# Optimization experiments

Hardware: AMD Instinct MI355X
Metric: run time of the kernel (lower is better)

Reference implementation:

```python
import jax, jax.numpy as jnp
import numpy as np

IN, OUT, IO, CF, CS = 128, 128, 512, 512, 1024
B = 8192
TAU_IO, TAU_CF, TAU_CS = 2.0, 5.0, 70.0


def _lin(x, W, b):
    # torch nn.Linear: y = x @ W.T + b, W has shape [out, in]
    return x @ W.T + b


def setup_inputs() -> dict:
    key = jax.random.key(0)
    ks = jax.random.split(key, 24)

    def wb(i, fan_out, fan_in):
        s = 1.0 / np.sqrt(fan_in)
        W = jax.random.uniform(ks[2 * i], (fan_out, fan_in), jnp.float32, -s, s)
        b = jax.random.uniform(ks[2 * i + 1], (fan_out,), jnp.float32, -s, s)
        return W, b

    Wi2io, bi2io = wb(0, IO, IN)
    Wio2o, bio2o = wb(1, OUT, IO)
    Wio2io, bio2io = wb(2, IO, IO)
    Wio2cf, bio2cf = wb(3, CF, IO)
    Wcf2io, bcf2io = wb(4, IO, CF)
    Wcf2cs, bcf2cs = wb(5, CS, CF)
    Wcf2cf, bcf2cf = wb(6, CF, CF)
    Wcs2cf, bcs2cf = wb(7, CF, CS)
    Wcs2cs, bcs2cs = wb(8, CS, CS)

    x = jax.random.normal(ks[18], (B, IN), jnp.float32)
    io_state = jnp.zeros((B, IO), jnp.float32)
    cf_state = jnp.zeros((B, CF), jnp.float32)
    cs_state = jnp.zeros((B, CS), jnp.float32)

    return dict(
        x=x, io_state=io_state, cf_state=cf_state, cs_state=cs_state,
        Wi2io=Wi2io, bi2io=bi2io, Wio2o=Wio2o, bio2o=bio2o,
        Wio2io=Wio2io, bio2io=bio2io, Wio2cf=Wio2cf, bio2cf=bio2cf,
        Wcf2io=Wcf2io, bcf2io=bcf2io, Wcf2cs=Wcf2cs, bcf2cs=bcf2cs,
        Wcf2cf=Wcf2cf, bcf2cf=bcf2cf, Wcs2cf=Wcs2cf, bcs2cf=bcs2cf,
        Wcs2cs=Wcs2cs, bcs2cs=bcs2cs,
    )


def reference(x, io_state, cf_state, cs_state,
              Wi2io, bi2io, Wio2o, bio2o,
              Wio2io, bio2io, Wio2cf, bio2cf,
              Wcf2io, bcf2io, Wcf2cs, bcf2cs,
              Wcf2cf, bcf2cf, Wcs2cf, bcs2cf,
              Wcs2cs, bcs2cs):
    x = x.reshape(-1, IN)
    # leaky-integrated updates; all branches read the *previous* states
    io_new = jnp.tanh(
        (1.0 - 1.0 / TAU_IO) * io_state
        + (_lin(io_state, Wio2io, bio2io)
           + _lin(cf_state, Wcf2io, bcf2io)
           + _lin(x, Wi2io, bi2io)) / TAU_IO)
    cf_new = jnp.tanh(
        (1.0 - 1.0 / TAU_CF) * cf_state
        + (_lin(cf_state, Wcf2cf, bcf2cf)
           + _lin(cs_state, Wcs2cf, bcs2cf)
           + _lin(io_state, Wio2cf, bio2cf)) / TAU_CF)
    cs_new = jnp.tanh(
        (1.0 - 1.0 / TAU_CS) * cs_state
        + (_lin(cs_state, Wcs2cs, bcs2cs)
           + _lin(cf_state, Wcf2cs, bcf2cs)) / TAU_CS)
    y = jnp.tanh(_lin(io_new, Wio2o, bio2o))
    return y
```

## Files before the change

### kernel.cpp

```cpp
#include <hip/hip_runtime.h>


typedef float f32x4 __attribute__((ext_vector_type(4)));
typedef __bf16 bf16x4 __attribute__((ext_vector_type(4)));
typedef __bf16 bf16x8 __attribute__((ext_vector_type(8)));
typedef unsigned short u16x4 __attribute__((ext_vector_type(4)));

__device__ __forceinline__ unsigned short f2bf(float f) {
    unsigned u = __builtin_bit_cast(unsigned, f);
    u += 0x7FFFu + ((u >> 16) & 1u);
    return (unsigned short)(u >> 16);
}

__device__ __forceinline__ float tanh_fast(float x) {
    float e = __expf(2.0f * x);
    return 1.0f - 2.0f * __builtin_amdgcn_rcpf(e + 1.0f);
}

__device__ __forceinline__ void gload16(const void* g, void* l) {
    __builtin_amdgcn_global_load_lds(
        (const __attribute__((address_space(1))) void*)g,
        (__attribute__((address_space(3))) void*)l, 16, 0, 0);
}

#define WAITB(N) asm volatile("s_waitcnt vmcnt(" #N ")\n\ts_barrier" ::: "memory")

__device__ __forceinline__ int swz_ad(int row, int k, int L) {
    return row * L + (k & ~63) + ((((k >> 3) & 7) ^ (row & 7)) << 3) + (k & 7);
}

__global__ __launch_bounds__(256) void k_prep(
    const float* __restrict__ x, const float* __restrict__ io,
    const float* __restrict__ cf,
    const float* __restrict__ Wi2io, const float* __restrict__ Wio2io,
    const float* __restrict__ Wcf2io, const float* __restrict__ Wio2o,
    const float* __restrict__ b1, const float* __restrict__ b2,
    const float* __restrict__ b3,
    unsigned short* __restrict__ abf16, unsigned short* __restrict__ wcat,
    unsigned short* __restrict__ w2s, float* __restrict__ bsum)
{
    int idx = blockIdx.x * 256 + threadIdx.x;
    if (idx < 1179648) {
        int m = idx / 144;
        int k = (idx - m * 144) * 8;
        const float* s;
        if (k < 128)      s = x  + m * 128 + k;
        else if (k < 640) s = io + m * 512 + (k - 128);
        else              s = cf + m * 512 + (k - 640);
        f32x4 v0 = *(const f32x4*)s;
        f32x4 v1 = *(const f32x4*)(s + 4);
        bf16x4 h0 = __builtin_convertvector(v0, bf16x4);
        bf16x4 h1 = __builtin_convertvector(v1, bf16x4);
        *(bf16x8*)(abf16 + swz_ad(m, k, 1152)) =
            __builtin_shufflevector(h0, h1, 0,1,2,3,4,5,6,7);
    } else if (idx < 1253376) {
        int q = idx - 1179648;
        int n = q / 144;
        int k = (q - n * 144) * 8;
        const float* s;
        if (k < 128)      s = Wi2io  + n * 128 + k;
        else if (k < 640) s = Wio2io + n * 512 + (k - 128);
        else              s = Wcf2io + n * 512 + (k - 640);
        f32x4 v0 = *(const f32x4*)s;
        f32x4 v1 = *(const f32x4*)(s + 4);
        float w[8];
        #pragma unroll
        for (int t = 0; t < 4; ++t) { w[t] = 0.5f * v0[t]; w[t+4] = 0.5f * v1[t]; }
        #pragma unroll
        for (int t = 0; t < 8; ++t) {
            int kk = k + t;
            if (kk >= 128 && kk < 640 && (kk - 128) == n) w[t] += 0.5f;
        }
        unsigned short* dst = wcat + swz_ad(n, k, 1152);
        #pragma unroll
        for (int t = 0; t < 8; ++t) dst[t] = f2bf(w[t]);
    } else if (idx < 1261568) {
        int q = idx - 1253376;
        int n = q >> 6;
        int k = (q & 63) * 8;
        f32x4 v0 = *(const f32x4*)(Wio2o + n * 512 + k);
        f32x4 v1 = *(const f32x4*)(Wio2o + n * 512 + k + 4);
        bf16x4 h0 = __builtin_convertvector(v0, bf16x4);
        bf16x4 h1 = __builtin_convertvector(v1, bf16x4);
        *(bf16x8*)(w2s + swz_ad(n, k, 512)) =
            __builtin_shufflevector(h0, h1, 0,1,2,3,4,5,6,7);
    } else if (idx < 1262080) {
        int n = idx - 1261568;
        bsum[n] = 0.5f * (b1[n] + b2[n] + b3[n]);
    }
}

__global__ __launch_bounds__(512, 2) void k_gemm1(
    const unsigned short* __restrict__ abf16,
    const unsigned short* __restrict__ wcat,
    const float* __restrict__ bsum,
    unsigned short* __restrict__ ionew)
{
    __shared__ __align__(16) char lds[3][32768];

    const int tid = threadIdx.x, b = blockIdx.x;
    const int xcd = b & 7, idx = b >> 3;
    const int m0 = ((xcd << 3) | (idx & 7)) << 7;
    const int n0 = (idx >> 3) << 7;

    const int lane = tid & 63, wid = tid >> 6;
    const int li = lane & 15, lh = lane >> 4;
    const int wm = (wid >> 1) << 5;
    const int wn = (wid & 1) << 6;

    int a_off[2], b_off[2];
    #pragma unroll
    for (int j = 0; j < 2; ++j) {
        int ra = (wid << 4) + (j << 3) + (lane >> 3);
        a_off[j] = (m0 + ra) * 1152 + ((lane & 7) << 3);
        int rb = (wid << 4) + (j << 3) + (lane >> 3);
        b_off[j] = (n0 + rb) * 1152 + ((lane & 7) << 3);
    }
    const int adst = wid << 11;

    f32x4 zz = {0.f, 0.f, 0.f, 0.f};
    f32x4 acc[2][4];
    #pragma unroll
    for (int i = 0; i < 2; ++i)
        #pragma unroll
        for (int j = 0; j < 4; ++j) acc[i][j] = zz;

#define STAGE1(KT, BUF) do {                                                   \
        int K_ = (KT);                                                         \
        char* A_ = (BUF); char* B_ = (BUF) + 16384;                            \
        const unsigned short* ap = abf16 + (K_ << 6);                          \
        gload16(ap + a_off[0], A_ + adst);                                     \
        gload16(ap + a_off[1], A_ + adst + 1024);                              \
        const unsigned short* wp = wcat + (K_ << 6);                           \
        gload16(wp + b_off[0], B_ + adst);                                     \
        gload16(wp + b_off[1], B_ + adst + 1024);                              \
    } while (0)

#define COMPUTE1(BUF) do {                                                     \
        const char* A_ = (BUF); const char* B_ = (BUF) + 16384;                \
        _Pragma("unroll")                                                      \
        for (int ks = 0; ks < 2; ++ks) {                                       \
            int c = ks * 4 + lh;                                               \
            bf16x8 af[2];                                                      \
            _Pragma("unroll")                                                  \
            for (int mi = 0; mi < 2; ++mi) {                                   \
                int r = wm + mi * 16 + li;                                     \
                af[mi] = *(const bf16x8*)(A_ + r * 128 + ((c ^ (r & 7)) << 4));\
            }                                                                  \
            _Pragma("unroll")                                                  \
            for (int nj = 0; nj < 4; ++nj) {                                   \
                int rb = wn + nj * 16 + li;                                    \
                bf16x8 bv = *(const bf16x8*)(B_ + rb * 128 +                   \
                                             ((c ^ (rb & 7)) << 4));           \
                acc[0][nj] = __builtin_amdgcn_mfma_f32_16x16x32_bf16(          \
                    af[0], bv, acc[0][nj], 0, 0, 0);                           \
                acc[1][nj] = __builtin_amdgcn_mfma_f32_16x16x32_bf16(          \
                    af[1], bv, acc[1][nj], 0, 0, 0);                           \
            }                                                                  \
        }                                                                      \
    } while (0)

    STAGE1(0, lds[0]);
    STAGE1(1, lds[1]);
    char* p0 = lds[0]; char* p1 = lds[1]; char* p2 = lds[2];
    #pragma unroll 1
    for (int t = 0; t < 18; ++t) {
        if (t < 17) { WAITB(4); } else { WAITB(0); }
        if (t + 2 < 18) STAGE1(t + 2, p2);
        COMPUTE1(p0);
        char* tmp = p0; p0 = p1; p1 = p2; p2 = tmp;
    }
#undef STAGE1
#undef COMPUTE1

    #pragma unroll
    for (int nj = 0; nj < 4; ++nj) {
        int gn = n0 + wn + nj * 16 + li;
        float bb = bsum[gn];
        #pragma unroll
        for (int mi = 0; mi < 2; ++mi) {
            #pragma unroll
            for (int r = 0; r < 4; ++r) {
                int gm = m0 + wm + mi * 16 + (lh << 2) + r;
                float v = tanh_fast(acc[mi][nj][r] + bb);
                ionew[swz_ad(gm, gn, 512)] = f2bf(v);
            }
        }
    }
}

__global__ __launch_bounds__(256, 2) void k_gemm2(
    const unsigned short* __restrict__ ionew,
    const unsigned short* __restrict__ w2s,
    const float* __restrict__ b4,
    float* __restrict__ out)
{
    __shared__ __align__(16) char lds[3][20480];

    const int tid = threadIdx.x, b = blockIdx.x;
    const int xcd = b & 7, idx = b >> 3;
    const int m0 = ((xcd << 5) | idx) << 5;

    const int lane = tid & 63, wid = tid >> 6;
    const int li = lane & 15, lh = lane >> 4;
    const int wn = wid << 5;

    const int a2_off = (m0 + (wid << 3) + (lane >> 3)) * 512 + ((lane & 7) << 3);
    int b2_off[4];
    #pragma unroll
    for (int j = 0; j < 4; ++j)
        b2_off[j] = ((wid << 5) + 8 * j + (lane >> 3)) * 512 + ((lane & 7) << 3);

    f32x4 zz = {0.f, 0.f, 0.f, 0.f};
    f32x4 acc[2][2];
    acc[0][0] = zz; acc[0][1] = zz; acc[1][0] = zz; acc[1][1] = zz;

#define STAGE2(KT, BUF) do {                                                   \
        int K_ = (KT);                                                         \
        char* A_ = (BUF); char* B_ = (BUF) + 4096;                             \
        gload16(ionew + a2_off + (K_ << 6), A_ + (wid << 10));                 \
        _Pragma("unroll")                                                      \
        for (int j = 0; j < 4; ++j)                                            \
            gload16(w2s + b2_off[j] + (K_ << 6), B_ + (wid << 12) + j * 1024); \
    } while (0)

#define COMPUTE2(BUF) do {                                                     \
        const char* A_ = (BUF); const char* B_ = (BUF) + 4096;                 \
        _Pragma("unroll")                                                      \
        for (int ks = 0; ks < 2; ++ks) {                                       \
            int c = ks * 4 + lh;                                               \
            bf16x8 av[2];                                                      \
            _Pragma("unroll")                                                  \
            for (int mi = 0; mi < 2; ++mi) {                                   \
                int r = mi * 16 + li;                                          \
                av[mi] = *(const bf16x8*)(A_ + r * 128 + ((c ^ (r & 7)) << 4));\
            }                                                                  \
            _Pragma("unroll")                                                  \
            for (int nj = 0; nj < 2; ++nj) {                                   \
                int rb = wn + nj * 16 + li;                                    \
                bf16x8 bv = *(const bf16x8*)(B_ + rb * 128 +                   \
                                             ((c ^ (rb & 7)) << 4));           \
                acc[0][nj] = __builtin_amdgcn_mfma_f32_16x16x32_bf16(          \
                    av[0], bv, acc[0][nj], 0, 0, 0);                           \
                acc[1][nj] = __builtin_amdgcn_mfma_f32_16x16x32_bf16(          \
                    av[1], bv, acc[1][nj], 0, 0, 0);                           \
            }                                                                  \
        }                                                                      \
    } while (0)

    STAGE2(0, lds[0]);
    STAGE2(1, lds[1]);
    char* p0 = lds[0]; char* p1 = lds[1]; char* p2 = lds[2];
    #pragma unroll 1
    for (int t = 0; t < 7; ++t) {
        WAITB(5);
        if (t + 2 < 8) STAGE2(t + 2, p2);
        COMPUTE2(p0);
        char* tmp = p0; p0 = p1; p1 = p2; p2 = tmp;
    }
    WAITB(0);
    COMPUTE2(p0);
#undef STAGE2
#undef COMPUTE2

    #pragma unroll
    for (int nj = 0; nj < 2; ++nj) {
        int n = wn + nj * 16 + li;
        float bb = b4[n];
        #pragma unroll
        for (int mi = 0; mi < 2; ++mi) {
            #pragma unroll
            for (int r = 0; r < 4; ++r) {
                int gm = m0 + mi * 16 + (lh << 2) + r;
                out[(size_t)gm * 128 + n] = tanh_fast(acc[mi][nj][r] + bb);
            }
        }
    }
}

extern "C" void kernel_launch(void* const* d_in, const int* in_sizes, int n_in,
                              void* d_out, int out_size, void* d_ws, size_t ws_size,
                              hipStream_t stream)
{
    const float* x      = (const float*)d_in[0];
    const float* io     = (const float*)d_in[1];
    const float* cf     = (const float*)d_in[2];
    const float* Wi2io  = (const float*)d_in[4];
    const float* bi2io  = (const float*)d_in[5];
    const float* Wio2o  = (const float*)d_in[6];
    const float* bio2o  = (const float*)d_in[7];
    const float* Wio2io = (const float*)d_in[8];
    const float* bio2io = (const float*)d_in[9];
    const float* Wcf2io = (const float*)d_in[12];
    const float* bcf2io = (const float*)d_in[13];
    float* out = (float*)d_out;

    char* ws = (char*)d_ws;
    unsigned short* abf16 = (unsigned short*)ws;
    unsigned short* wcat  = (unsigned short*)(ws + 18874368);
    unsigned short* w2s   = (unsigned short*)(ws + 20054016);
    float*          bsum  = (float*)(ws + 20185088);
    unsigned short* ionew = (unsigned short*)(ws + 20187136);

    hipLaunchKernelGGL(k_prep, dim3(4930), dim3(256), 0, stream,
                       x, io, cf, Wi2io, Wio2io, Wcf2io, Wio2o,
                       bi2io, bio2io, bcf2io, abf16, wcat, w2s, bsum);
    hipLaunchKernelGGL(k_gemm1, dim3(256), dim3(512), 0, stream,
                       abf16, wcat, bsum, ionew);
    hipLaunchKernelGGL(k_gemm2, dim3(256), dim3(256), 0, stream,
                       ionew, w2s, bio2o, out);
}
```

Before: 33.47 us.

## Pre-layout B weights in MFMA fragment order and load directly to registers

The prep kernel now writes the concatenated io weight matrix in a per-fragment layout, so each lane can load its MFMA B operand with one 16-byte global load. The GEMM1 kernel stops staging B through LDS, halves its LDS buffers, and loads B fragments into registers each K-step. It also raises wave priority around the MFMA block. This cuts LDS traffic and the B-side LDS reads, but B loads now go to global/L2 with no LDS sharing between waves, and their latency is exposed inside each iteration.

```diff
diff --git a/kernel.cpp b/kernel.cpp
--- a/kernel.cpp
+++ b/kernel.cpp
@@ -36,7 +36,7 @@
     const float* __restrict__ Wcf2io, const float* __restrict__ Wio2o,
     const float* __restrict__ b1, const float* __restrict__ b2,
     const float* __restrict__ b3,
-    unsigned short* __restrict__ abf16, unsigned short* __restrict__ wcat,
+    unsigned short* __restrict__ abf16, unsigned short* __restrict__ wfrag,
     unsigned short* __restrict__ w2s, float* __restrict__ bsum)
 {
     int idx = blockIdx.x * 256 + threadIdx.x;
@@ -71,7 +71,9 @@
             int kk = k + t;
             if (kk >= 128 && kk < 640 && (kk - 128) == n) w[t] += 0.5f;
         }
-        unsigned short* dst = wcat + swz_ad(n, k, 1152);
+        int kt = k >> 6, ks = (k >> 5) & 1, c16 = n >> 4;
+        int l = (n & 15) | (((k >> 3) & 3) << 4);
+        unsigned short* dst = wfrag + ((((kt << 5) | c16) << 1) | ks) * 512 + l * 8;
         #pragma unroll
         for (int t = 0; t < 8; ++t) dst[t] = f2bf(w[t]);
     } else if (idx < 1261568) {
@@ -92,11 +94,11 @@
 
 __global__ __launch_bounds__(512, 2) void k_gemm1(
     const unsigned short* __restrict__ abf16,
-    const unsigned short* __restrict__ wcat,
+    const unsigned short* __restrict__ wfrag,
     const float* __restrict__ bsum,
     unsigned short* __restrict__ ionew)
 {
-    __shared__ __align__(16) char lds[3][32768];
+    __shared__ __align__(16) char lds[3][16384];
 
     const int tid = threadIdx.x, b = blockIdx.x;
     const int xcd = b & 7, idx = b >> 3;
@@ -108,15 +110,15 @@
     const int wm = (wid >> 1) << 5;
     const int wn = (wid & 1) << 6;
 
-    int a_off[2], b_off[2];
+    int a_off[2];
     #pragma unroll
     for (int j = 0; j < 2; ++j) {
         int ra = (wid << 4) + (j << 3) + (lane >> 3);
         a_off[j] = (m0 + ra) * 1152 + ((lane & 7) << 3);
-        int rb = (wid << 4) + (j << 3) + (lane >> 3);
-        b_off[j] = (n0 + rb) * 1152 + ((lane & 7) << 3);
     }
     const int adst = wid << 11;
+
+    const unsigned short* fb = wfrag + ((n0 + wn) >> 4) * 1024 + lane * 8;
 
     f32x4 zz = {0.f, 0.f, 0.f, 0.f};
     f32x4 acc[2][4];
@@ -124,20 +126,26 @@
     for (int i = 0; i < 2; ++i)
         #pragma unroll
         for (int j = 0; j < 4; ++j) acc[i][j] = zz;
-
-#define STAGE1(KT, BUF) do {                                                   \
-        int K_ = (KT);                                                         \
-        char* A_ = (BUF); char* B_ = (BUF) + 16384;                            \
-        const unsigned short* ap = abf16 + (K_ << 6);                          \
+    bf16x8 Bv[4][2];
+
+#define ASTAGE(KT, BUF) do {                                                   \
+        char* A_ = (BUF);                                                      \
+        const unsigned short* ap = abf16 + ((KT) << 6);                        \
         gload16(ap + a_off[0], A_ + adst);                                     \
         gload16(ap + a_off[1], A_ + adst + 1024);                              \
-        const unsigned short* wp = wcat + (K_ << 6);                           \
-        gload16(wp + b_off[0], B_ + adst);                                     \
-        gload16(wp + b_off[1], B_ + adst + 1024);                              \
+    } while (0)
+
+#define BLOAD(KT) do {                                                         \
+        const unsigned short* fp = fb + (size_t)(KT) * 32768;                  \
+        _Pragma("unroll")                                                      \
+        for (int nj = 0; nj < 4; ++nj)                                         \
+            _Pragma("unroll")                                                  \
+            for (int ks = 0; ks < 2; ++ks)                                     \
+                Bv[nj][ks] = *(const bf16x8*)(fp + nj * 1024 + ks * 512);      \
     } while (0)
 
 #define COMPUTE1(BUF) do {                                                     \
-        const char* A_ = (BUF); const char* B_ = (BUF) + 16384;                \
+        const char* A_ = (BUF);                                                \
         _Pragma("unroll")                                                      \
         for (int ks = 0; ks < 2; ++ks) {                                       \
             int c = ks * 4 + lh;                                               \
@@ -147,30 +155,31 @@
                 int r = wm + mi * 16 + li;                                     \
                 af[mi] = *(const bf16x8*)(A_ + r * 128 + ((c ^ (r & 7)) << 4));\
             }                                                                  \
+            __builtin_amdgcn_s_setprio(1);                                     \
             _Pragma("unroll")                                                  \
             for (int nj = 0; nj < 4; ++nj) {                                   \
-                int rb = wn + nj * 16 + li;                                    \
-                bf16x8 bv = *(const bf16x8*)(B_ + rb * 128 +                   \
-                                             ((c ^ (rb & 7)) << 4));           \
                 acc[0][nj] = __builtin_amdgcn_mfma_f32_16x16x32_bf16(          \
-                    af[0], bv, acc[0][nj], 0, 0, 0);                           \
+                    af[0], Bv[nj][ks], acc[0][nj], 0, 0, 0);                   \
                 acc[1][nj] = __builtin_amdgcn_mfma_f32_16x16x32_bf16(          \
-                    af[1], bv, acc[1][nj], 0, 0, 0);                           \
+                    af[1], Bv[nj][ks], acc[1][nj], 0, 0, 0);                   \
             }                                                                  \
+            __builtin_amdgcn_s_setprio(0);                                     \
         }                                                                      \
     } while (0)
 
-    STAGE1(0, lds[0]);
-    STAGE1(1, lds[1]);
+    ASTAGE(0, lds[0]);
+    ASTAGE(1, lds[1]);
     char* p0 = lds[0]; char* p1 = lds[1]; char* p2 = lds[2];
     #pragma unroll 1
     for (int t = 0; t < 18; ++t) {
-        if (t < 17) { WAITB(4); } else { WAITB(0); }
-        if (t + 2 < 18) STAGE1(t + 2, p2);
+        if (t < 17) { WAITB(2); } else { WAITB(0); }
+        BLOAD(t);
+        if (t + 2 < 18) ASTAGE(t + 2, p2);
         COMPUTE1(p0);
         char* tmp = p0; p0 = p1; p1 = p2; p2 = tmp;
     }
-#undef STAGE1
+#undef ASTAGE
+#undef BLOAD
 #undef COMPUTE1
 
     #pragma unroll
@@ -297,16 +306,16 @@
 
     char* ws = (char*)d_ws;
     unsigned short* abf16 = (unsigned short*)ws;
-    unsigned short* wcat  = (unsigned short*)(ws + 18874368);
+    unsigned short* wfrag = (unsigned short*)(ws + 18874368);
     unsigned short* w2s   = (unsigned short*)(ws + 20054016);
     float*          bsum  = (float*)(ws + 20185088);
     unsigned short* ionew = (unsigned short*)(ws + 20187136);
 
     hipLaunchKernelGGL(k_prep, dim3(4930), dim3(256), 0, stream,
                        x, io, cf, Wi2io, Wio2io, Wcf2io, Wio2o,
-                       bi2io, bio2io, bcf2io, abf16, wcat, w2s, bsum);
+                       bi2io, bio2io, bcf2io, abf16, wfrag, w2s, bsum);
     hipLaunchKernelGGL(k_gemm1, dim3(256), dim3(512), 0, stream,
-                       abf16, wcat, bsum, ionew);
+                       abf16, wfrag, bsum, ionew);
     hipLaunchKernelGGL(k_gemm2, dim3(256), dim3(256), 0, stream,
                        ionew, w2s, bio2o, out);
 }
```

Result: slower. 42.30 us (+26.4%).
